# Kernel tuning notes

Measured on AMD Instinct MI355X. Metric: run time of the kernel, lower is better.

The kernel has to match this reference:

```python
import jax, jax.numpy as jnp
import numpy as np

N_NODES = 50000
N_EDGES = 800000
IN_CH = 64
EDGE_DIM = 8
HIDDEN = 128
NUM_GRAPHS = 256


def setup_inputs() -> dict:
    key = jax.random.key(0)
    ks = jax.random.split(key, 16)
    x = jax.random.normal(ks[0], (N_NODES, IN_CH), dtype=jnp.float32)
    edge_index = jax.random.randint(ks[1], (2, N_EDGES), 0, N_NODES, dtype=jnp.int64)
    edge_attr = jax.random.normal(ks[2], (N_EDGES, EDGE_DIM), dtype=jnp.float32)
    batch = jnp.sort(jax.random.randint(ks[3], (N_NODES,), 0, NUM_GRAPHS, dtype=jnp.int64))

    def lin(k, fan_in, fan_out):
        bound = 1.0 / np.sqrt(fan_in)
        kw, kb = jax.random.split(k)
        W = jax.random.uniform(kw, (fan_in, fan_out), minval=-bound, maxval=bound, dtype=jnp.float32)
        b = jax.random.uniform(kb, (fan_out,), minval=-bound, maxval=bound, dtype=jnp.float32)
        return W, b

    W1, b1 = lin(ks[4], IN_CH, HIDDEN)
    We1, be1 = lin(ks[5], EDGE_DIM, IN_CH)
    W2, b2 = lin(ks[6], HIDDEN, HIDDEN)
    We2, be2 = lin(ks[7], EDGE_DIM, HIDDEN)
    W3, b3 = lin(ks[8], HIDDEN, HIDDEN)
    We3, be3 = lin(ks[9], EDGE_DIM, HIDDEN)
    return {"x": x, "edge_index": edge_index, "edge_attr": edge_attr, "batch": batch,
            "W1": W1, "b1": b1, "We1": We1, "be1": be1,
            "W2": W2, "b2": b2, "We2": We2, "be2": be2,
            "W3": W3, "b3": b3, "We3": We3, "be3": be3}


def gine_conv(x, src, dst, edge_attr, W, b, We, be):
    # edge feature projection to node-feature dim, then message = relu(x_j + e)
    e = edge_attr @ We + be                      # [E, d]
    msg = jax.nn.relu(x[src] + e)                # [E, d]
    agg = jax.ops.segment_sum(msg, dst, num_segments=x.shape[0])  # [N, d]
    # eps = 0 (PyG default, not trainable)
    return (x + agg) @ W + b


def reference(x, edge_index, edge_attr, batch,
              W1, b1, We1, be1, W2, b2, We2, be2, W3, b3, We3, be3):
    x = x.astype(jnp.float32)
    edge_attr = edge_attr.astype(jnp.float32)
    src, dst = edge_index[0], edge_index[1]
    x = jax.nn.relu(gine_conv(x, src, dst, edge_attr, W1, b1, We1, be1))
    x = jax.nn.relu(gine_conv(x, src, dst, edge_attr, W2, b2, We2, be2))
    x = jax.nn.relu(gine_conv(x, src, dst, edge_attr, W3, b3, We3, be3))
    # global mean pool over graphs
    sums = jax.ops.segment_sum(x, batch, num_segments=NUM_GRAPHS)          # [G, d]
    counts = jax.ops.segment_sum(jnp.ones((x.shape[0],), x.dtype), batch, num_segments=NUM_GRAPHS)
    return sums / jnp.maximum(counts, 1.0)[:, None]
```

## Files before the change

### kernel.cpp

```cpp
#include <hip/hip_runtime.h>
#include <hip/hip_bf16.h>
#include <hip/hip_fp16.h>

#define N_NODES 50000
#define N_EDGES 800000
#define IN_CH 64
#define EDGE_DIM 8
#define HIDDEN 128
#define NUM_GRAPHS 256
#define NPASS 2
#define PASS_W ((N_NODES + NPASS - 1) / NPASS)
#define QSCALE 256.0f
#define QINV   (1.0f / 256.0f)

typedef __attribute__((ext_vector_type(8))) _Float16 half8;
typedef __attribute__((ext_vector_type(4))) float floatx4;
typedef __attribute__((ext_vector_type(2))) float floatx2;
typedef __attribute__((ext_vector_type(4))) int intx4;

static __device__ __forceinline__ __half2 u2h(int u) {
    union { int i; __half2 h; } cv; cv.i = u; return cv.h;
}
static __device__ __forceinline__ int h2u(__half2 h) {
    union { __half2 h; int i; } cv; cv.h = h; return cv.i;
}
static __device__ __forceinline__ unsigned short h1u(__half h) {
    union { __half h; unsigned short u; } cv; cv.h = h; return cv.u;
}
static __device__ __forceinline__ unsigned char f32_to_fp8(float v) {
    int pk = __builtin_amdgcn_cvt_pk_fp8_f32(v, v, 0, false);
    return (unsigned char)(pk & 0xff);
}

__global__ __launch_bounds__(256) void hist_kernel(
    const int* __restrict__ dst, int* __restrict__ deg, int E)
{
    int i = blockIdx.x * blockDim.x + threadIdx.x;
    if (i < E) atomicAdd(&deg[dst[i]], 1);
}

__global__ __launch_bounds__(256) void scan1_kernel(
    const int* __restrict__ deg, int* __restrict__ incl,
    int* __restrict__ blockSums, int N)
{
    __shared__ int s[256];
    int b = blockIdx.x, t = threadIdx.x;
    int i0 = b * 512 + 2 * t;
    int a0 = (i0 < N) ? deg[i0] : 0;
    int a1 = (i0 + 1 < N) ? deg[i0 + 1] : 0;
    int ps = a0 + a1;
    s[t] = ps;
    __syncthreads();
    for (int off = 1; off < 256; off <<= 1) {
        int v = (t >= off) ? s[t - off] : 0;
        __syncthreads();
        s[t] += v;
        __syncthreads();
    }
    int exclp = s[t] - ps;
    if (i0 < N)     incl[i0]     = exclp + a0;
    if (i0 + 1 < N) incl[i0 + 1] = exclp + a0 + a1;
    if (t == 255) blockSums[b] = s[255];
}

__global__ __launch_bounds__(128) void scan2_kernel(int* __restrict__ blockSums, int B)
{
    __shared__ int s[128];
    int t = threadIdx.x;
    int v = (t < B) ? blockSums[t] : 0;
    s[t] = v;
    __syncthreads();
    for (int off = 1; off < 128; off <<= 1) {
        int u = (t >= off) ? s[t - off] : 0;
        __syncthreads();
        s[t] += u;
        __syncthreads();
    }
    if (t < B) blockSums[t] = s[t] - v;
}

__global__ __launch_bounds__(256) void scan3_kernel(
    const int* __restrict__ incl, const int* __restrict__ deg,
    const int* __restrict__ blockSums, int* __restrict__ rowptr,
    int* __restrict__ pos, int N)
{
    int i = blockIdx.x * blockDim.x + threadIdx.x;
    if (i >= N) return;
    int v = incl[i] - deg[i] + blockSums[i >> 9];
    rowptr[i] = v;
    pos[i] = v;
}

__global__ __launch_bounds__(256) void scatter_rec_kernel(
    const int* __restrict__ dst, const int* __restrict__ src,
    const float* __restrict__ ea, int* __restrict__ pos,
    int* __restrict__ src_s, __half* __restrict__ ea16, int lo, int E)
{
    int e = blockIdx.x * blockDim.x + threadIdx.x;
    if (e >= E) return;
    int d = dst[e];
    if ((unsigned)(d - lo) >= (unsigned)PASS_W) return;
    int p = atomicAdd(&pos[d], 1);
    __builtin_nontemporal_store(src[e], &src_s[p]);
    const float4* q = (const float4*)(ea + (size_t)e * EDGE_DIM);
    float4 a = q[0], b = q[1];
    intx4 r;
    r.x = h2u(__floats2half2_rn(a.x, a.y));
    r.y = h2u(__floats2half2_rn(a.z, a.w));
    r.z = h2u(__floats2half2_rn(b.x, b.y));
    r.w = h2u(__floats2half2_rn(b.z, b.w));
    __builtin_nontemporal_store(r, (intx4*)(ea16 + (size_t)p * EDGE_DIM));
}

#define XH_ELEMS (N_NODES * IN_CH)
__global__ __launch_bounds__(256) void cvt_all_kernel(
    const float* __restrict__ x, unsigned char* __restrict__ xh8,
    const float* __restrict__ W1, const float* __restrict__ W2,
    const float* __restrict__ W3,
    _Float16* __restrict__ Wt1, _Float16* __restrict__ Wt2,
    _Float16* __restrict__ Wt3)
{
    int idx = blockIdx.x * blockDim.x + threadIdx.x;
    if (idx < XH_ELEMS) { xh8[idx] = f32_to_fp8(x[idx]); return; }
    idx -= XH_ELEMS;
    if (idx < 128 * IN_CH) {
        int n = idx / IN_CH, k = idx - n * IN_CH;
        Wt1[idx] = (_Float16)W1[k * 128 + n];
        return;
    }
    idx -= 128 * IN_CH;
    if (idx < 128 * HIDDEN) {
        int n = idx / HIDDEN, k = idx - n * HIDDEN;
        Wt2[idx] = (_Float16)W2[k * 128 + n];
        return;
    }
    idx -= 128 * HIDDEN;
    if (idx < 128 * HIDDEN) {
        int n = idx / HIDDEN, k = idx - n * HIDDEN;
        Wt3[idx] = (_Float16)W3[k * 128 + n];
    }
}

#define BF 8

__global__ __launch_bounds__(256) void gather_xs128_kernel(
    const unsigned char* __restrict__ h8,
    const int*    __restrict__ src_s,
    const __half* __restrict__ ea16,
    const int*    __restrict__ rowptr,
    const int*    __restrict__ deg,
    const float*  __restrict__ We,
    const float*  __restrict__ be,
    __half*       __restrict__ xs,
    int N)
{
    int wave = threadIdx.x >> 6;
    int n    = blockIdx.x * 4 + wave;
    if (n >= N) return;
    int l  = threadIdx.x & 63;
    int j0 = 2 * l;

    __half2 hw[8];
    #pragma unroll
    for (int k = 0; k < 8; ++k) {
        float2 wv = *(const float2*)&We[k * 128 + j0];
        hw[k] = __floats2half2_rn(wv.x, wv.y);
    }
    float2 bevf = *(const float2*)&be[j0];
    __half2 bev2 = __floats2half2_rn(bevf.x, bevf.y);

    int start = __builtin_amdgcn_readfirstlane(rowptr[n]);
    int dg    = __builtin_amdgcn_readfirstlane(deg[n]);

    unsigned short selfraw = *(const unsigned short*)&h8[(size_t)n * 128 + j0];
    floatx2 hf = __builtin_amdgcn_cvt_pk_f32_fp8((int)selfraw, false);
    int acci0 = 0, acci1 = 0;

    int nb = dg / BF;
    int base = start;
    for (int b = 0; b < nb; ++b, base += BF) {
        int sid[BF];
        #pragma unroll
        for (int t = 0; t < BF; ++t)
            sid[t] = __builtin_amdgcn_readfirstlane(
                __builtin_nontemporal_load(&src_s[base + t]));
        unsigned short hraw[BF];
        #pragma unroll
        for (int t = 0; t < BF; ++t)
            hraw[t] = *(const unsigned short*)&h8[(size_t)sid[t] * 128 + j0];
        intx4 eav[BF];
        #pragma unroll
        for (int t = 0; t < BF; ++t)
            eav[t] = __builtin_nontemporal_load(
                (const intx4*)&ea16[(size_t)(base + t) * 8]);

        #pragma unroll
        for (int t = 0; t < BF; ++t) {
            __half2 e01 = u2h(eav[t].x), e23 = u2h(eav[t].y);
            __half2 e45 = u2h(eav[t].z), e67 = u2h(eav[t].w);
            __half2 m = __hfma2(__low2half2(e01),  hw[0], bev2);
            m = __hfma2(__high2half2(e01), hw[1], m);
            m = __hfma2(__low2half2(e23),  hw[2], m);
            m = __hfma2(__high2half2(e23), hw[3], m);
            m = __hfma2(__low2half2(e45),  hw[4], m);
            m = __hfma2(__high2half2(e45), hw[5], m);
            m = __hfma2(__low2half2(e67),  hw[6], m);
            m = __hfma2(__high2half2(e67), hw[7], m);
            floatx2 hs = __builtin_amdgcn_cvt_pk_f32_fp8((int)hraw[t], false);
            float m0 = __half2float(__low2half(m))  + hs.x;
            float m1 = __half2float(__high2half(m)) + hs.y;
            acci0 += (int)((m0 > 0.0f ? m0 : 0.0f) * QSCALE);
            acci1 += (int)((m1 > 0.0f ? m1 : 0.0f) * QSCALE);
        }
    }
    int end = start + dg;
    for (int idx = base; idx < end; ++idx) {
        int s = __builtin_amdgcn_readfirstlane(src_s[idx]);
        unsigned short hr = *(const unsigned short*)&h8[(size_t)s * 128 + j0];
        intx4 ev = __builtin_nontemporal_load((const intx4*)&ea16[(size_t)idx * 8]);
        __half2 e01 = u2h(ev.x), e23 = u2h(ev.y), e45 = u2h(ev.z), e67 = u2h(ev.w);
        __half2 m = __hfma2(__low2half2(e01),  hw[0], bev2);
        m = __hfma2(__high2half2(e01), hw[1], m);
        m = __hfma2(__low2half2(e23),  hw[2], m);
        m = __hfma2(__high2half2(e23), hw[3], m);
        m = __hfma2(__low2half2(e45),  hw[4], m);
        m = __hfma2(__high2half2(e45), hw[5], m);
        m = __hfma2(__low2half2(e67),  hw[6], m);
        m = __hfma2(__high2half2(e67), hw[7], m);
        floatx2 hs = __builtin_amdgcn_cvt_pk_f32_fp8((int)hr, false);
        float m0 = __half2float(__low2half(m))  + hs.x;
        float m1 = __half2float(__high2half(m)) + hs.y;
        acci0 += (int)((m0 > 0.0f ? m0 : 0.0f) * QSCALE);
        acci1 += (int)((m1 > 0.0f ? m1 : 0.0f) * QSCALE);
    }
    float acc0 = hf.x + (float)acci0 * QINV;
    float acc1 = hf.y + (float)acci1 * QINV;
    __builtin_nontemporal_store(h2u(__floats2half2_rn(acc0, acc1)),
                                (int*)&xs[(size_t)n * 128 + j0]);
}

__global__ __launch_bounds__(256) void gather_xs64_kernel(
    const unsigned char* __restrict__ h8,
    const int*    __restrict__ src_s,
    const __half* __restrict__ ea16,
    const int*    __restrict__ rowptr,
    const int*    __restrict__ deg,
    const float*  __restrict__ We,
    const float*  __restrict__ be,
    __half*       __restrict__ xs,
    int N)
{
    int wave = threadIdx.x >> 6;
    int n    = blockIdx.x * 4 + wave;
    if (n >= N) return;
    int j = threadIdx.x & 63;

    __half2 w2[4];
    #pragma unroll
    for (int p = 0; p < 4; ++p)
        w2[p] = __floats2half2_rn(We[(2 * p) * 64 + j], We[(2 * p + 1) * 64 + j]);
    float bej = be[j];

    int start = __builtin_amdgcn_readfirstlane(rowptr[n]);
    int dg    = __builtin_amdgcn_readfirstlane(deg[n]);

    float selff = __builtin_amdgcn_cvt_f32_fp8((int)h8[(size_t)n * 64 + j], 0);
    int acci = 0;

    int nb = dg / BF;
    int base = start;
    for (int b = 0; b < nb; ++b, base += BF) {
        int sid[BF];
        #pragma unroll
        for (int t = 0; t < BF; ++t)
            sid[t] = __builtin_amdgcn_readfirstlane(
                __builtin_nontemporal_load(&src_s[base + t]));
        unsigned char hraw[BF];
        #pragma unroll
        for (int t = 0; t < BF; ++t)
            hraw[t] = h8[(size_t)sid[t] * 64 + j];
        intx4 eav[BF];
        #pragma unroll
        for (int t = 0; t < BF; ++t)
            eav[t] = __builtin_nontemporal_load(
                (const intx4*)&ea16[(size_t)(base + t) * 8]);

        #pragma unroll
        for (int t = 0; t < BF; ++t) {
            __half2 d = __hmul2(u2h(eav[t].x), w2[0]);
            d = __hfma2(u2h(eav[t].y), w2[1], d);
            d = __hfma2(u2h(eav[t].z), w2[2], d);
            d = __hfma2(u2h(eav[t].w), w2[3], d);
            float proj = __half2float(__low2half(d)) + __half2float(__high2half(d));
            float hrf = __builtin_amdgcn_cvt_f32_fp8((int)hraw[t], 0);
            float m = hrf + proj + bej;
            acci += (int)((m > 0.0f ? m : 0.0f) * QSCALE);
        }
    }
    int end = start + dg;
    for (int idx = base; idx < end; ++idx) {
        int s = __builtin_amdgcn_readfirstlane(src_s[idx]);
        float hrf = __builtin_amdgcn_cvt_f32_fp8((int)h8[(size_t)s * 64 + j], 0);
        intx4 ev = __builtin_nontemporal_load((const intx4*)&ea16[(size_t)idx * 8]);
        __half2 d = __hmul2(u2h(ev.x), w2[0]);
        d = __hfma2(u2h(ev.y), w2[1], d);
        d = __hfma2(u2h(ev.z), w2[2], d);
        d = __hfma2(u2h(ev.w), w2[3], d);
        float proj = __half2float(__low2half(d)) + __half2float(__high2half(d));
        float m = hrf + proj + bej;
        acci += (int)((m > 0.0f ? m : 0.0f) * QSCALE);
    }
    float acc = selff + (float)acci * QINV;
    __builtin_nontemporal_store(h1u(__float2half(acc)),
                                (unsigned short*)&xs[(size_t)n * 64 + j]);
}

template<int K, bool OUT8>
__global__ __launch_bounds__(256) void node_mfma_kernel(
    const _Float16* __restrict__ xs,
    const _Float16* __restrict__ Wt,
    const float*    __restrict__ b,
    _Float16*       __restrict__ out16,
    unsigned char*  __restrict__ out8,
    int N)
{
    int wave  = threadIdx.x >> 6;
    int lane  = threadIdx.x & 63;
    int row16 = lane & 15;
    int quad  = lane >> 4;
    int m0    = (blockIdx.x * 4 + wave) * 32;

    int nA = m0 + row16;        if (nA >= N) nA = N - 1;
    int nB = m0 + 16 + row16;   if (nB >= N) nB = N - 1;

    floatx4 accA[8], accB[8];
    #pragma unroll
    for (int t = 0; t < 8; ++t) { accA[t] = (floatx4)(0.0f); accB[t] = (floatx4)(0.0f); }

    #pragma unroll
    for (int kc = 0; kc < K; kc += 32) {
        half8 a0 = __builtin_nontemporal_load((const half8*)&xs[(size_t)nA * K + kc + quad * 8]);
        half8 a1 = __builtin_nontemporal_load((const half8*)&xs[(size_t)nB * K + kc + quad * 8]);
        #pragma unroll
        for (int t = 0; t < 8; ++t) {
            half8 bf = *(const half8*)&Wt[(size_t)(t * 16 + row16) * K + kc + quad * 8];
            accA[t] = __builtin_amdgcn_mfma_f32_16x16x32_f16(a0, bf, accA[t], 0, 0, 0);
            accB[t] = __builtin_amdgcn_mfma_f32_16x16x32_f16(a1, bf, accB[t], 0, 0, 0);
        }
    }

    #pragma unroll
    for (int t = 0; t < 8; ++t) {
        int col = t * 16 + row16;
        float bj = b[col];
        #pragma unroll
        for (int r = 0; r < 4; ++r) {
            int nodeA = m0 + quad * 4 + r;
            if (nodeA < N) {
                float v = accA[t][r] + bj;
                v = v > 0.0f ? v : 0.0f;
                if (OUT8) out8[(size_t)nodeA * 128 + col] = f32_to_fp8(v);
                else      out16[(size_t)nodeA * 128 + col] = (_Float16)v;
            }
            int nodeB = m0 + 16 + quad * 4 + r;
            if (nodeB < N) {
                float v = accB[t][r] + bj;
                v = v > 0.0f ? v : 0.0f;
                if (OUT8) out8[(size_t)nodeB * 128 + col] = f32_to_fp8(v);
                else      out16[(size_t)nodeB * 128 + col] = (_Float16)v;
            }
        }
    }
}

__global__ __launch_bounds__(256) void pool_kernel(
    const __half* __restrict__ h,
    const int*    __restrict__ batch,
    float*        __restrict__ out,
    int N)
{
    __shared__ int s_lo, s_hi;
    __shared__ float part[4][128];
    int g  = blockIdx.x;
    int t  = threadIdx.x;
    int fp = t & 63;
    int r  = t >> 6;

    if (t == 0) {
        int lo = 0, hi = N;
        while (lo < hi) { int m = (lo + hi) >> 1; if (batch[m] < g) lo = m + 1; else hi = m; }
        s_lo = lo;
        int lo2 = lo, hi2 = N;
        while (lo2 < hi2) { int m = (lo2 + hi2) >> 1; if (batch[m] < g + 1) lo2 = m + 1; else hi2 = m; }
        s_hi = lo2;
    }
    __syncthreads();

    int lo = s_lo, hi = s_hi;
    float a0 = 0.0f, a1 = 0.0f;
    for (int n = lo + r; n < hi; n += 4) {
        float2 f = __half22float2(*(const __half2*)&h[(size_t)n * 128 + 2 * fp]);
        a0 += f.x; a1 += f.y;
    }
    part[r][2 * fp]     = a0;
    part[r][2 * fp + 1] = a1;
    __syncthreads();

    if (r == 0) {
        float s0 = part[0][2 * fp] + part[1][2 * fp] + part[2][2 * fp] + part[3][2 * fp];
        float s1 = part[0][2 * fp + 1] + part[1][2 * fp + 1] + part[2][2 * fp + 1] + part[3][2 * fp + 1];
        float c = (float)(hi - lo);
        float d = c > 1.0f ? c : 1.0f;
        out[g * HIDDEN + 2 * fp]     = s0 / d;
        out[g * HIDDEN + 2 * fp + 1] = s1 / d;
    }
}

extern "C" void kernel_launch(void* const* d_in, const int* in_sizes, int n_in,
                              void* d_out, int out_size, void* d_ws, size_t ws_size,
                              hipStream_t stream)
{
    const float* x   = (const float*)d_in[0];
    const int*   ei  = (const int*)d_in[1];
    const float* ea  = (const float*)d_in[2];
    const int*   bat = (const int*)d_in[3];
    const float* W1  = (const float*)d_in[4];
    const float* b1  = (const float*)d_in[5];
    const float* We1 = (const float*)d_in[6];
    const float* be1 = (const float*)d_in[7];
    const float* W2  = (const float*)d_in[8];
    const float* b2  = (const float*)d_in[9];
    const float* We2 = (const float*)d_in[10];
    const float* be2 = (const float*)d_in[11];
    const float* W3  = (const float*)d_in[12];
    const float* b3  = (const float*)d_in[13];
    const float* We3 = (const float*)d_in[14];
    const float* be3 = (const float*)d_in[15];
    float* out = (float*)d_out;

    const int* src = ei;
    const int* dst = ei + N_EDGES;

    int* deg       = (int*)d_ws;
    int* rowptr    = deg + N_NODES;
    int* pos       = rowptr + N_NODES;
    int* src_s     = pos + N_NODES;
    int* blockSums = src_s + N_EDGES;
    __half* ea16   = (__half*)(blockSums + 128);
    __half* xs     = ea16 + (size_t)N_EDGES * EDGE_DIM;
    __half* h3h    = xs + (size_t)N_NODES * HIDDEN;
    unsigned char* xh8  = (unsigned char*)(h3h + (size_t)N_NODES * HIDDEN);
    unsigned char* h1_8 = xh8 + (size_t)N_NODES * IN_CH;
    unsigned char* h2_8 = h1_8 + (size_t)N_NODES * HIDDEN;
    _Float16* Wt1  = (_Float16*)(h2_8 + (size_t)N_NODES * HIDDEN);
    _Float16* Wt2  = Wt1 + 128 * IN_CH;
    _Float16* Wt3  = Wt2 + 128 * HIDDEN;

    const int BLK = 256;
    const int NB_E = (N_EDGES + BLK - 1) / BLK;
    const int NB_N = (N_NODES + BLK - 1) / BLK;
    const int SCAN_B = (N_NODES + 511) / 512;
    const int MFMA_B = (N_NODES + 127) / 128;
    const int WAVE4_B = (N_NODES + 3) / 4;
    const int CVT_ELEMS = XH_ELEMS + 128 * IN_CH + 2 * 128 * HIDDEN;

    (void)hipMemsetAsync(deg, 0, N_NODES * sizeof(int), stream);
    hist_kernel<<<NB_E, BLK, 0, stream>>>(dst, deg, N_EDGES);
    scan1_kernel<<<SCAN_B, 256, 0, stream>>>(deg, pos, blockSums, N_NODES);
    scan2_kernel<<<1, 128, 0, stream>>>(blockSums, SCAN_B);
    scan3_kernel<<<NB_N, BLK, 0, stream>>>(pos, deg, blockSums, rowptr, pos, N_NODES);
    for (int pass = 0; pass < NPASS; ++pass) {
        scatter_rec_kernel<<<NB_E, BLK, 0, stream>>>(
            dst, src, ea, pos, src_s, ea16, pass * PASS_W, N_EDGES);
    }
    cvt_all_kernel<<<(CVT_ELEMS + BLK - 1) / BLK, BLK, 0, stream>>>(
        x, xh8, W1, W2, W3, Wt1, Wt2, Wt3);

    gather_xs64_kernel<<<WAVE4_B, BLK, 0, stream>>>(
        xh8, src_s, ea16, rowptr, deg, We1, be1, xs, N_NODES);
    node_mfma_kernel<IN_CH, true><<<MFMA_B, 256, 0, stream>>>(
        (const _Float16*)xs, Wt1, b1, nullptr, h1_8, N_NODES);

    gather_xs128_kernel<<<WAVE4_B, BLK, 0, stream>>>(
        h1_8, src_s, ea16, rowptr, deg, We2, be2, xs, N_NODES);
    node_mfma_kernel<HIDDEN, true><<<MFMA_B, 256, 0, stream>>>(
        (const _Float16*)xs, Wt2, b2, nullptr, h2_8, N_NODES);

    gather_xs128_kernel<<<WAVE4_B, BLK, 0, stream>>>(
        h2_8, src_s, ea16, rowptr, deg, We3, be3, xs, N_NODES);
    node_mfma_kernel<HIDDEN, false><<<MFMA_B, 256, 0, stream>>>(
        (const _Float16*)xs, Wt3, b3, (_Float16*)h3h, nullptr, N_NODES);

    pool_kernel<<<NUM_GRAPHS, 256, 0, stream>>>(h3h, bat, out, N_NODES);
}
```

Measured before the change: 419.6 us.

## Fuse edge gather with per-layer MFMA linear via LDS tile, merge hist and convert

Each layer's neighbor aggregation and its dense linear transform now run in one kernel: a block aggregates 32 nodes into an LDS tile, then four waves compute MFMA output slices from it. This removes the global xs intermediate write/read and several kernel launches. The degree histogram is also folded into the conversion kernel. The trade-off is fewer, longer-running blocks, with each wave processing 8 nodes serially, which may reduce latency hiding for the irregular gathers.

```diff
diff --git a/kernel.cpp b/kernel.cpp
--- a/kernel.cpp
+++ b/kernel.cpp
@@ -24,19 +24,42 @@
 static __device__ __forceinline__ int h2u(__half2 h) {
     union { __half2 h; int i; } cv; cv.h = h; return cv.i;
 }
-static __device__ __forceinline__ unsigned short h1u(__half h) {
-    union { __half h; unsigned short u; } cv; cv.h = h; return cv.u;
-}
 static __device__ __forceinline__ unsigned char f32_to_fp8(float v) {
     int pk = __builtin_amdgcn_cvt_pk_fp8_f32(v, v, 0, false);
     return (unsigned char)(pk & 0xff);
 }
 
-__global__ __launch_bounds__(256) void hist_kernel(
-    const int* __restrict__ dst, int* __restrict__ deg, int E)
+#define XH_ELEMS (N_NODES * IN_CH)
+
+__global__ __launch_bounds__(256) void hist_cvt_kernel(
+    const int* __restrict__ dst, int* __restrict__ deg,
+    const float* __restrict__ x, unsigned char* __restrict__ xh8,
+    const float* __restrict__ W1, const float* __restrict__ W2,
+    const float* __restrict__ W3,
+    _Float16* __restrict__ Wt1, _Float16* __restrict__ Wt2,
+    _Float16* __restrict__ Wt3, int E)
 {
     int i = blockIdx.x * blockDim.x + threadIdx.x;
     if (i < E) atomicAdd(&deg[dst[i]], 1);
+    int idx = i;
+    if (idx < XH_ELEMS) { xh8[idx] = f32_to_fp8(x[idx]); return; }
+    idx -= XH_ELEMS;
+    if (idx < 128 * IN_CH) {
+        int n = idx / IN_CH, k = idx - n * IN_CH;
+        Wt1[idx] = (_Float16)W1[k * 128 + n];
+        return;
+    }
+    idx -= 128 * IN_CH;
+    if (idx < 128 * HIDDEN) {
+        int n = idx / HIDDEN, k = idx - n * HIDDEN;
+        Wt2[idx] = (_Float16)W2[k * 128 + n];
+        return;
+    }
+    idx -= 128 * HIDDEN;
+    if (idx < 128 * HIDDEN) {
+        int n = idx / HIDDEN, k = idx - n * HIDDEN;
+        Wt3[idx] = (_Float16)W3[k * 128 + n];
+    }
 }
 
 __global__ __launch_bounds__(256) void scan1_kernel(
@@ -112,38 +135,10 @@
     __builtin_nontemporal_store(r, (intx4*)(ea16 + (size_t)p * EDGE_DIM));
 }
 
-#define XH_ELEMS (N_NODES * IN_CH)
-__global__ __launch_bounds__(256) void cvt_all_kernel(
-    const float* __restrict__ x, unsigned char* __restrict__ xh8,
-    const float* __restrict__ W1, const float* __restrict__ W2,
-    const float* __restrict__ W3,
-    _Float16* __restrict__ Wt1, _Float16* __restrict__ Wt2,
-    _Float16* __restrict__ Wt3)
-{
-    int idx = blockIdx.x * blockDim.x + threadIdx.x;
-    if (idx < XH_ELEMS) { xh8[idx] = f32_to_fp8(x[idx]); return; }
-    idx -= XH_ELEMS;
-    if (idx < 128 * IN_CH) {
-        int n = idx / IN_CH, k = idx - n * IN_CH;
-        Wt1[idx] = (_Float16)W1[k * 128 + n];
-        return;
-    }
-    idx -= 128 * IN_CH;
-    if (idx < 128 * HIDDEN) {
-        int n = idx / HIDDEN, k = idx - n * HIDDEN;
-        Wt2[idx] = (_Float16)W2[k * 128 + n];
-        return;
-    }
-    idx -= 128 * HIDDEN;
-    if (idx < 128 * HIDDEN) {
-        int n = idx / HIDDEN, k = idx - n * HIDDEN;
-        Wt3[idx] = (_Float16)W3[k * 128 + n];
-    }
-}
-
 #define BF 8
 
-__global__ __launch_bounds__(256) void gather_xs128_kernel(
+template<int K, bool OUT8>
+__global__ __launch_bounds__(256) void layer_fused_kernel(
     const unsigned char* __restrict__ h8,
     const int*    __restrict__ src_s,
     const __half* __restrict__ ea16,
@@ -151,220 +146,203 @@
     const int*    __restrict__ deg,
     const float*  __restrict__ We,
     const float*  __restrict__ be,
-    __half*       __restrict__ xs,
+    const _Float16* __restrict__ Wt,
+    const float*  __restrict__ bias,
+    _Float16*     __restrict__ out16,
+    unsigned char* __restrict__ out8,
     int N)
 {
+    __shared__ _Float16 xsl[32][K + 8];
     int wave = threadIdx.x >> 6;
-    int n    = blockIdx.x * 4 + wave;
-    if (n >= N) return;
-    int l  = threadIdx.x & 63;
-    int j0 = 2 * l;
-
-    __half2 hw[8];
+    int l    = threadIdx.x & 63;
+    int m0   = blockIdx.x * 32;
+
+    if constexpr (K == 128) {
+        int j0 = 2 * l;
+        __half2 hw[8];
+        #pragma unroll
+        for (int k = 0; k < 8; ++k) {
+            float2 wv = *(const float2*)&We[k * 128 + j0];
+            hw[k] = __floats2half2_rn(wv.x, wv.y);
+        }
+        float2 bevf = *(const float2*)&be[j0];
+        __half2 bev2 = __floats2half2_rn(bevf.x, bevf.y);
+
+        for (int i = 0; i < 8; ++i) {
+            int nl = wave * 8 + i;
+            int n  = m0 + nl;
+            if (n >= N) { *(__half2*)&xsl[nl][j0] = __floats2half2_rn(0.f, 0.f); continue; }
+
+            int start = __builtin_amdgcn_readfirstlane(rowptr[n]);
+            int dg    = __builtin_amdgcn_readfirstlane(deg[n]);
+
+            unsigned short selfraw = *(const unsigned short*)&h8[(size_t)n * 128 + j0];
+            floatx2 hf = __builtin_amdgcn_cvt_pk_f32_fp8((int)selfraw, false);
+            int acci0 = 0, acci1 = 0;
+
+            int nb = dg / BF;
+            int base = start;
+            for (int b = 0; b < nb; ++b, base += BF) {
+                int sid[BF];
+                #pragma unroll
+                for (int t = 0; t < BF; ++t)
+                    sid[t] = __builtin_amdgcn_readfirstlane(
+                        __builtin_nontemporal_load(&src_s[base + t]));
+                unsigned short hraw[BF];
+                #pragma unroll
+                for (int t = 0; t < BF; ++t)
+                    hraw[t] = *(const unsigned short*)&h8[(size_t)sid[t] * 128 + j0];
+                intx4 eav[BF];
+                #pragma unroll
+                for (int t = 0; t < BF; ++t)
+                    eav[t] = __builtin_nontemporal_load(
+                        (const intx4*)&ea16[(size_t)(base + t) * 8]);
+
+                #pragma unroll
+                for (int t = 0; t < BF; ++t) {
+                    __half2 e01 = u2h(eav[t].x), e23 = u2h(eav[t].y);
+                    __half2 e45 = u2h(eav[t].z), e67 = u2h(eav[t].w);
+                    __half2 m = __hfma2(__low2half2(e01),  hw[0], bev2);
+                    m = __hfma2(__high2half2(e01), hw[1], m);
+                    m = __hfma2(__low2half2(e23),  hw[2], m);
+                    m = __hfma2(__high2half2(e23), hw[3], m);
+                    m = __hfma2(__low2half2(e45),  hw[4], m);
+                    m = __hfma2(__high2half2(e45), hw[5], m);
+                    m = __hfma2(__low2half2(e67),  hw[6], m);
+                    m = __hfma2(__high2half2(e67), hw[7], m);
+                    floatx2 hs = __builtin_amdgcn_cvt_pk_f32_fp8((int)hraw[t], false);
+                    float m0f = __half2float(__low2half(m))  + hs.x;
+                    float m1f = __half2float(__high2half(m)) + hs.y;
+                    acci0 += (int)((m0f > 0.0f ? m0f : 0.0f) * QSCALE);
+                    acci1 += (int)((m1f > 0.0f ? m1f : 0.0f) * QSCALE);
+                }
+            }
+            int end = start + dg;
+            for (int idx = base; idx < end; ++idx) {
+                int s = __builtin_amdgcn_readfirstlane(src_s[idx]);
+                unsigned short hr = *(const unsigned short*)&h8[(size_t)s * 128 + j0];
+                intx4 ev = __builtin_nontemporal_load((const intx4*)&ea16[(size_t)idx * 8]);
+                __half2 e01 = u2h(ev.x), e23 = u2h(ev.y), e45 = u2h(ev.z), e67 = u2h(ev.w);
+                __half2 m = __hfma2(__low2half2(e01),  hw[0], bev2);
+                m = __hfma2(__high2half2(e01), hw[1], m);
+                m = __hfma2(__low2half2(e23),  hw[2], m);
+                m = __hfma2(__high2half2(e23), hw[3], m);
+                m = __hfma2(__low2half2(e45),  hw[4], m);
+                m = __hfma2(__high2half2(e45), hw[5], m);
+                m = __hfma2(__low2half2(e67),  hw[6], m);
+                m = __hfma2(__high2half2(e67), hw[7], m);
+                floatx2 hs = __builtin_amdgcn_cvt_pk_f32_fp8((int)hr, false);
+                float m0f = __half2float(__low2half(m))  + hs.x;
+                float m1f = __half2float(__high2half(m)) + hs.y;
+                acci0 += (int)((m0f > 0.0f ? m0f : 0.0f) * QSCALE);
+                acci1 += (int)((m1f > 0.0f ? m1f : 0.0f) * QSCALE);
+            }
+            float acc0 = hf.x + (float)acci0 * QINV;
+            float acc1 = hf.y + (float)acci1 * QINV;
+            *(__half2*)&xsl[nl][j0] = __floats2half2_rn(acc0, acc1);
+        }
+    } else {
+        int j = l;
+        __half2 w2[4];
+        #pragma unroll
+        for (int p = 0; p < 4; ++p)
+            w2[p] = __floats2half2_rn(We[(2 * p) * 64 + j], We[(2 * p + 1) * 64 + j]);
+        float bej = be[j];
+
+        for (int i = 0; i < 8; ++i) {
+            int nl = wave * 8 + i;
+            int n  = m0 + nl;
+            if (n >= N) { xsl[nl][j] = (_Float16)0.0f; continue; }
+
+            int start = __builtin_amdgcn_readfirstlane(rowptr[n]);
+            int dg    = __builtin_amdgcn_readfirstlane(deg[n]);
+
+            float selff = __builtin_amdgcn_cvt_f32_fp8((int)h8[(size_t)n * 64 + j], 0);
+            int acci = 0;
+
+            int nb = dg / BF;
+            int base = start;
+            for (int b = 0; b < nb; ++b, base += BF) {
+                int sid[BF];
+                #pragma unroll
+                for (int t = 0; t < BF; ++t)
+                    sid[t] = __builtin_amdgcn_readfirstlane(
+                        __builtin_nontemporal_load(&src_s[base + t]));
+                unsigned char hraw[BF];
+                #pragma unroll
+                for (int t = 0; t < BF; ++t)
+                    hraw[t] = h8[(size_t)sid[t] * 64 + j];
+                intx4 eav[BF];
+                #pragma unroll
+                for (int t = 0; t < BF; ++t)
+                    eav[t] = __builtin_nontemporal_load(
+                        (const intx4*)&ea16[(size_t)(base + t) * 8]);
+
+                #pragma unroll
+                for (int t = 0; t < BF; ++t) {
+                    __half2 d = __hmul2(u2h(eav[t].x), w2[0]);
+                    d = __hfma2(u2h(eav[t].y), w2[1], d);
+                    d = __hfma2(u2h(eav[t].z), w2[2], d);
+                    d = __hfma2(u2h(eav[t].w), w2[3], d);
+                    float proj = __half2float(__low2half(d)) + __half2float(__high2half(d));
+                    float hrf = __builtin_amdgcn_cvt_f32_fp8((int)hraw[t], 0);
+                    float m = hrf + proj + bej;
+                    acci += (int)((m > 0.0f ? m : 0.0f) * QSCALE);
+                }
+            }
+            int end = start + dg;
+            for (int idx = base; idx < end; ++idx) {
+                int s = __builtin_amdgcn_readfirstlane(src_s[idx]);
+                float hrf = __builtin_amdgcn_cvt_f32_fp8((int)h8[(size_t)s * 64 + j], 0);
+                intx4 ev = __builtin_nontemporal_load((const intx4*)&ea16[(size_t)idx * 8]);
+                __half2 d = __hmul2(u2h(ev.x), w2[0]);
+                d = __hfma2(u2h(ev.y), w2[1], d);
+                d = __hfma2(u2h(ev.z), w2[2], d);
+                d = __hfma2(u2h(ev.w), w2[3], d);
+                float proj = __half2float(__low2half(d)) + __half2float(__high2half(d));
+                float m = hrf + proj + bej;
+                acci += (int)((m > 0.0f ? m : 0.0f) * QSCALE);
+            }
+            xsl[nl][j] = (_Float16)(selff + (float)acci * QINV);
+        }
+    }
+    __syncthreads();
+
+    int row16 = l & 15;
+    int quad  = l >> 4;
+    floatx4 accA[2], accB[2];
     #pragma unroll
-    for (int k = 0; k < 8; ++k) {
-        float2 wv = *(const float2*)&We[k * 128 + j0];
-        hw[k] = __floats2half2_rn(wv.x, wv.y);
-    }
-    float2 bevf = *(const float2*)&be[j0];
-    __half2 bev2 = __floats2half2_rn(bevf.x, bevf.y);
-
-    int start = __builtin_amdgcn_readfirstlane(rowptr[n]);
-    int dg    = __builtin_amdgcn_readfirstlane(deg[n]);
-
-    unsigned short selfraw = *(const unsigned short*)&h8[(size_t)n * 128 + j0];
-    floatx2 hf = __builtin_amdgcn_cvt_pk_f32_fp8((int)selfraw, false);
-    int acci0 = 0, acci1 = 0;
-
-    int nb = dg / BF;
-    int base = start;
-    for (int b = 0; b < nb; ++b, base += BF) {
-        int sid[BF];
-        #pragma unroll
-        for (int t = 0; t < BF; ++t)
-            sid[t] = __builtin_amdgcn_readfirstlane(
-                __builtin_nontemporal_load(&src_s[base + t]));
-        unsigned short hraw[BF];
-        #pragma unroll
-        for (int t = 0; t < BF; ++t)
-            hraw[t] = *(const unsigned short*)&h8[(size_t)sid[t] * 128 + j0];
-        intx4 eav[BF];
-        #pragma unroll
-        for (int t = 0; t < BF; ++t)
-            eav[t] = __builtin_nontemporal_load(
-                (const intx4*)&ea16[(size_t)(base + t) * 8]);
-
-        #pragma unroll
-        for (int t = 0; t < BF; ++t) {
-            __half2 e01 = u2h(eav[t].x), e23 = u2h(eav[t].y);
-            __half2 e45 = u2h(eav[t].z), e67 = u2h(eav[t].w);
-            __half2 m = __hfma2(__low2half2(e01),  hw[0], bev2);
-            m = __hfma2(__high2half2(e01), hw[1], m);
-            m = __hfma2(__low2half2(e23),  hw[2], m);
-            m = __hfma2(__high2half2(e23), hw[3], m);
-            m = __hfma2(__low2half2(e45),  hw[4], m);
-            m = __hfma2(__high2half2(e45), hw[5], m);
-            m = __hfma2(__low2half2(e67),  hw[6], m);
-            m = __hfma2(__high2half2(e67), hw[7], m);
-            floatx2 hs = __builtin_amdgcn_cvt_pk_f32_fp8((int)hraw[t], false);
-            float m0 = __half2float(__low2half(m))  + hs.x;
-            float m1 = __half2float(__high2half(m)) + hs.y;
-            acci0 += (int)((m0 > 0.0f ? m0 : 0.0f) * QSCALE);
-            acci1 += (int)((m1 > 0.0f ? m1 : 0.0f) * QSCALE);
-        }
-    }
-    int end = start + dg;
-    for (int idx = base; idx < end; ++idx) {
-        int s = __builtin_amdgcn_readfirstlane(src_s[idx]);
-        unsigned short hr = *(const unsigned short*)&h8[(size_t)s * 128 + j0];
-        intx4 ev = __builtin_nontemporal_load((const intx4*)&ea16[(size_t)idx * 8]);
-        __half2 e01 = u2h(ev.x), e23 = u2h(ev.y), e45 = u2h(ev.z), e67 = u2h(ev.w);
-        __half2 m = __hfma2(__low2half2(e01),  hw[0], bev2);
-        m = __hfma2(__high2half2(e01), hw[1], m);
-        m = __hfma2(__low2half2(e23),  hw[2], m);
-        m = __hfma2(__high2half2(e23), hw[3], m);
-        m = __hfma2(__low2half2(e45),  hw[4], m);
-        m = __hfma2(__high2half2(e45), hw[5], m);
-        m = __hfma2(__low2half2(e67),  hw[6], m);
-        m = __hfma2(__high2half2(e67), hw[7], m);
-        floatx2 hs = __builtin_amdgcn_cvt_pk_f32_fp8((int)hr, false);
-        float m0 = __half2float(__low2half(m))  + hs.x;
-        float m1 = __half2float(__high2half(m)) + hs.y;
-        acci0 += (int)((m0 > 0.0f ? m0 : 0.0f) * QSCALE);
-        acci1 += (int)((m1 > 0.0f ? m1 : 0.0f) * QSCALE);
-    }
-    float acc0 = hf.x + (float)acci0 * QINV;
-    float acc1 = hf.y + (float)acci1 * QINV;
-    __builtin_nontemporal_store(h2u(__floats2half2_rn(acc0, acc1)),
-                                (int*)&xs[(size_t)n * 128 + j0]);
-}
-
-__global__ __launch_bounds__(256) void gather_xs64_kernel(
-    const unsigned char* __restrict__ h8,
-    const int*    __restrict__ src_s,
-    const __half* __restrict__ ea16,
-    const int*    __restrict__ rowptr,
-    const int*    __restrict__ deg,
-    const float*  __restrict__ We,
-    const float*  __restrict__ be,
-    __half*       __restrict__ xs,
-    int N)
-{
-    int wave = threadIdx.x >> 6;
-    int n    = blockIdx.x * 4 + wave;
-    if (n >= N) return;
-    int j = threadIdx.x & 63;
-
-    __half2 w2[4];
-    #pragma unroll
-    for (int p = 0; p < 4; ++p)
-        w2[p] = __floats2half2_rn(We[(2 * p) * 64 + j], We[(2 * p + 1) * 64 + j]);
-    float bej = be[j];
-
-    int start = __builtin_amdgcn_readfirstlane(rowptr[n]);
-    int dg    = __builtin_amdgcn_readfirstlane(deg[n]);
-
-    float selff = __builtin_amdgcn_cvt_f32_fp8((int)h8[(size_t)n * 64 + j], 0);
-    int acci = 0;
-
-    int nb = dg / BF;
-    int base = start;
-    for (int b = 0; b < nb; ++b, base += BF) {
-        int sid[BF];
-        #pragma unroll
-        for (int t = 0; t < BF; ++t)
-            sid[t] = __builtin_amdgcn_readfirstlane(
-                __builtin_nontemporal_load(&src_s[base + t]));
-        unsigned char hraw[BF];
-        #pragma unroll
-        for (int t = 0; t < BF; ++t)
-            hraw[t] = h8[(size_t)sid[t] * 64 + j];
-        intx4 eav[BF];
-        #pragma unroll
-        for (int t = 0; t < BF; ++t)
-            eav[t] = __builtin_nontemporal_load(
-                (const intx4*)&ea16[(size_t)(base + t) * 8]);
-
-        #pragma unroll
-        for (int t = 0; t < BF; ++t) {
-            __half2 d = __hmul2(u2h(eav[t].x), w2[0]);
-            d = __hfma2(u2h(eav[t].y), w2[1], d);
-            d = __hfma2(u2h(eav[t].z), w2[2], d);
-            d = __hfma2(u2h(eav[t].w), w2[3], d);
-            float proj = __half2float(__low2half(d)) + __half2float(__high2half(d));
-            float hrf = __builtin_amdgcn_cvt_f32_fp8((int)hraw[t], 0);
-            float m = hrf + proj + bej;
-            acci += (int)((m > 0.0f ? m : 0.0f) * QSCALE);
-        }
-    }
-    int end = start + dg;
-    for (int idx = base; idx < end; ++idx) {
-        int s = __builtin_amdgcn_readfirstlane(src_s[idx]);
-        float hrf = __builtin_amdgcn_cvt_f32_fp8((int)h8[(size_t)s * 64 + j], 0);
-        intx4 ev = __builtin_nontemporal_load((const intx4*)&ea16[(size_t)idx * 8]);
-        __half2 d = __hmul2(u2h(ev.x), w2[0]);
-        d = __hfma2(u2h(ev.y), w2[1], d);
-        d = __hfma2(u2h(ev.z), w2[2], d);
-        d = __hfma2(u2h(ev.w), w2[3], d);
-        float proj = __half2float(__low2half(d)) + __half2float(__high2half(d));
-        float m = hrf + proj + bej;
-        acci += (int)((m > 0.0f ? m : 0.0f) * QSCALE);
-    }
-    float acc = selff + (float)acci * QINV;
-    __builtin_nontemporal_store(h1u(__float2half(acc)),
-                                (unsigned short*)&xs[(size_t)n * 64 + j]);
-}
-
-template<int K, bool OUT8>
-__global__ __launch_bounds__(256) void node_mfma_kernel(
-    const _Float16* __restrict__ xs,
-    const _Float16* __restrict__ Wt,
-    const float*    __restrict__ b,
-    _Float16*       __restrict__ out16,
-    unsigned char*  __restrict__ out8,
-    int N)
-{
-    int wave  = threadIdx.x >> 6;
-    int lane  = threadIdx.x & 63;
-    int row16 = lane & 15;
-    int quad  = lane >> 4;
-    int m0    = (blockIdx.x * 4 + wave) * 32;
-
-    int nA = m0 + row16;        if (nA >= N) nA = N - 1;
-    int nB = m0 + 16 + row16;   if (nB >= N) nB = N - 1;
-
-    floatx4 accA[8], accB[8];
-    #pragma unroll
-    for (int t = 0; t < 8; ++t) { accA[t] = (floatx4)(0.0f); accB[t] = (floatx4)(0.0f); }
+    for (int t2 = 0; t2 < 2; ++t2) { accA[t2] = (floatx4)(0.0f); accB[t2] = (floatx4)(0.0f); }
 
     #pragma unroll
     for (int kc = 0; kc < K; kc += 32) {
-        half8 a0 = __builtin_nontemporal_load((const half8*)&xs[(size_t)nA * K + kc + quad * 8]);
-        half8 a1 = __builtin_nontemporal_load((const half8*)&xs[(size_t)nB * K + kc + quad * 8]);
+        half8 a0 = *(const half8*)&xsl[row16][kc + quad * 8];
+        half8 a1 = *(const half8*)&xsl[16 + row16][kc + quad * 8];
         #pragma unroll
-        for (int t = 0; t < 8; ++t) {
+        for (int t2 = 0; t2 < 2; ++t2) {
+            int t = wave * 2 + t2;
             half8 bf = *(const half8*)&Wt[(size_t)(t * 16 + row16) * K + kc + quad * 8];
-            accA[t] = __builtin_amdgcn_mfma_f32_16x16x32_f16(a0, bf, accA[t], 0, 0, 0);
-            accB[t] = __builtin_amdgcn_mfma_f32_16x16x32_f16(a1, bf, accB[t], 0, 0, 0);
+            accA[t2] = __builtin_amdgcn_mfma_f32_16x16x32_f16(a0, bf, accA[t2], 0, 0, 0);
+            accB[t2] = __builtin_amdgcn_mfma_f32_16x16x32_f16(a1, bf, accB[t2], 0, 0, 0);
         }
     }
 
     #pragma unroll
-    for (int t = 0; t < 8; ++t) {
-        int col = t * 16 + row16;
-        float bj = b[col];
+    for (int t2 = 0; t2 < 2; ++t2) {
+        int col = (wave * 2 + t2) * 16 + row16;
+        float bj = bias[col];
         #pragma unroll
         for (int r = 0; r < 4; ++r) {
             int nodeA = m0 + quad * 4 + r;
             if (nodeA < N) {
-                float v = accA[t][r] + bj;
+                float v = accA[t2][r] + bj;
                 v = v > 0.0f ? v : 0.0f;
                 if (OUT8) out8[(size_t)nodeA * 128 + col] = f32_to_fp8(v);
                 else      out16[(size_t)nodeA * 128 + col] = (_Float16)v;
             }
             int nodeB = m0 + 16 + quad * 4 + r;
             if (nodeB < N) {
-                float v = accB[t][r] + bj;
+                float v = accB[t2][r] + bj;
                 v = v > 0.0f ? v : 0.0f;
                 if (OUT8) out8[(size_t)nodeB * 128 + col] = f32_to_fp8(v);
                 else      out16[(size_t)nodeB * 128 + col] = (_Float16)v;
@@ -447,8 +425,7 @@
     int* src_s     = pos + N_NODES;
     int* blockSums = src_s + N_EDGES;
     __half* ea16   = (__half*)(blockSums + 128);
-    __half* xs     = ea16 + (size_t)N_EDGES * EDGE_DIM;
-    __half* h3h    = xs + (size_t)N_NODES * HIDDEN;
+    __half* h3h    = ea16 + (size_t)N_EDGES * EDGE_DIM;
     unsigned char* xh8  = (unsigned char*)(h3h + (size_t)N_NODES * HIDDEN);
     unsigned char* h1_8 = xh8 + (size_t)N_NODES * IN_CH;
     unsigned char* h2_8 = h1_8 + (size_t)N_NODES * HIDDEN;
@@ -460,12 +437,13 @@
     const int NB_E = (N_EDGES + BLK - 1) / BLK;
     const int NB_N = (N_NODES + BLK - 1) / BLK;
     const int SCAN_B = (N_NODES + 511) / 512;
-    const int MFMA_B = (N_NODES + 127) / 128;
-    const int WAVE4_B = (N_NODES + 3) / 4;
+    const int FUSED_B = (N_NODES + 31) / 32;
     const int CVT_ELEMS = XH_ELEMS + 128 * IN_CH + 2 * 128 * HIDDEN;
+    const int NB_HC = (CVT_ELEMS + BLK - 1) / BLK;
 
     (void)hipMemsetAsync(deg, 0, N_NODES * sizeof(int), stream);
-    hist_kernel<<<NB_E, BLK, 0, stream>>>(dst, deg, N_EDGES);
+    hist_cvt_kernel<<<NB_HC, BLK, 0, stream>>>(
+        dst, deg, x, xh8, W1, W2, W3, Wt1, Wt2, Wt3, N_EDGES);
     scan1_kernel<<<SCAN_B, 256, 0, stream>>>(deg, pos, blockSums, N_NODES);
     scan2_kernel<<<1, 128, 0, stream>>>(blockSums, SCAN_B);
     scan3_kernel<<<NB_N, BLK, 0, stream>>>(pos, deg, blockSums, rowptr, pos, N_NODES);
@@ -473,23 +451,13 @@
         scatter_rec_kernel<<<NB_E, BLK, 0, stream>>>(
             dst, src, ea, pos, src_s, ea16, pass * PASS_W, N_EDGES);
     }
-    cvt_all_kernel<<<(CVT_ELEMS + BLK - 1) / BLK, BLK, 0, stream>>>(
-        x, xh8, W1, W2, W3, Wt1, Wt2, Wt3);
-
-    gather_xs64_kernel<<<WAVE4_B, BLK, 0, stream>>>(
-        xh8, src_s, ea16, rowptr, deg, We1, be1, xs, N_NODES);
-    node_mfma_kernel<IN_CH, true><<<MFMA_B, 256, 0, stream>>>(
-        (const _Float16*)xs, Wt1, b1, nullptr, h1_8, N_NODES);
-
-    gather_xs128_kernel<<<WAVE4_B, BLK, 0, stream>>>(
-        h1_8, src_s, ea16, rowptr, deg, We2, be2, xs, N_NODES);
-    node_mfma_kernel<HIDDEN, true><<<MFMA_B, 256, 0, stream>>>(
-        (const _Float16*)xs, Wt2, b2, nullptr, h2_8, N_NODES);
-
-    gather_xs128_kernel<<<WAVE4_B, BLK, 0, stream>>>(
-        h2_8, src_s, ea16, rowptr, deg, We3, be3, xs, N_NODES);
-    node_mfma_kernel<HIDDEN, false><<<MFMA_B, 256, 0, stream>>>(
-        (const _Float16*)xs, Wt3, b3, (_Float16*)h3h, nullptr, N_NODES);
+
+    layer_fused_kernel<IN_CH, true><<<FUSED_B, 256, 0, stream>>>(
+        xh8, src_s, ea16, rowptr, deg, We1, be1, Wt1, b1, nullptr, h1_8, N_NODES);
+    layer_fused_kernel<HIDDEN, true><<<FUSED_B, 256, 0, stream>>>(
+        h1_8, src_s, ea16, rowptr, deg, We2, be2, Wt2, b2, nullptr, h2_8, N_NODES);
+    layer_fused_kernel<HIDDEN, false><<<FUSED_B, 256, 0, stream>>>(
+        h2_8, src_s, ea16, rowptr, deg, We3, be3, Wt3, b3, (_Float16*)h3h, nullptr, N_NODES);
 
     pool_kernel<<<NUM_GRAPHS, 256, 0, stream>>>(h3h, bat, out, N_NODES);
 }
```

After: 420.5 us. About the same (+0.2%).
